# Kernel optimization log

Hardware: AMD Instinct MI355X
Metric: run time of the kernel (lower is better)

Reference implementation:

```python
import jax, jax.numpy as jnp
import numpy as np

B, S, D, H, I, E, K, L, C = 4, 1024, 512, 8, 2048, 8, 2, 4, 4
D2 = D // 2
EPS = 1e-5  # torch LayerNorm default


def _ln(x, w, b):
    m = jnp.mean(x, -1, keepdims=True)
    v = jnp.mean((x - m) ** 2, -1, keepdims=True)
    return (x - m) * jax.lax.rsqrt(v + EPS) * w + b


def setup_inputs() -> dict:
    key = jax.random.key(0)
    ks = iter(jax.random.split(key, 40))
    n = lambda shp, s=0.02: jax.random.normal(next(ks), shp, dtype=jnp.float32) * s
    return {
        'embeddings': jax.random.normal(next(ks), (B, S, D), jnp.float32),
        'attention_mask': jnp.ones((B, S), jnp.float32),
        'in_w': n((L, 3 * D, D)), 'in_b': jnp.zeros((L, 3 * D)),
        'out_w': n((L, D, D)), 'out_b': jnp.zeros((L, D)),
        'ln1_w': jnp.ones((L, D)), 'ln1_b': jnp.zeros((L, D)),
        'ln2_w': jnp.ones((L, D)), 'ln2_b': jnp.zeros((L, D)),
        'gate_w': n((L, E, D)),
        'e_w1': n((L, E, D, I)), 'e_b1': jnp.zeros((L, E, I)),
        'e_w2': n((L, E, I, D)), 'e_b2': jnp.zeros((L, E, D)),
        'mln_w': jnp.ones((L, D)), 'mln_b': jnp.zeros((L, D)),
        'fln_w': jnp.ones((D,)), 'fln_b': jnp.zeros((D,)),
        'pool_w': n((D, D)), 'pool_b': jnp.zeros((D,)),
        'cls_w': n((C, D)), 'cls_b': jnp.zeros((C,)),
        'cf_w1': n((D2, D)), 'cf_b1': jnp.zeros((D2,)),
        'cf_w2': n((1, D2)), 'cf_b2': jnp.zeros((1,)),
    }


def _forward(embeddings, attention_mask, in_w, in_b, out_w, out_b, ln1_w, ln1_b,
             ln2_w, ln2_b, gate_w, e_w1, e_b1, e_w2, e_b2, mln_w, mln_b,
             fln_w, fln_b, pool_w, pool_b, cls_w, cls_b, cf_w1, cf_b1, cf_w2, cf_b2):
    x = embeddings
    dh = D // H
    total_aux = jnp.float32(0.0)
    for l in range(L):
        # --- self-attention (eval mode, dropout off) ---
        h = _ln(x, ln1_w[l], ln1_b[l])
        qkv = h @ in_w[l].T + in_b[l]                       # (B,S,3D)
        q, k, v = jnp.split(qkv, 3, axis=-1)
        q = q.reshape(B, S, H, dh).transpose(0, 2, 1, 3)
        k = k.reshape(B, S, H, dh).transpose(0, 2, 1, 3)
        v = v.reshape(B, S, H, dh).transpose(0, 2, 1, 3)
        scores = jnp.einsum('bhqd,bhkd->bhqk', q, k) / (dh ** 0.5)
        attn = jax.nn.softmax(scores, axis=-1)
        ctx = jnp.einsum('bhqk,bhkd->bhqd', attn, v).transpose(0, 2, 1, 3).reshape(B, S, D)
        x = x + (ctx @ out_w[l].T + out_b[l])
        # --- MoE FFN (residual is the post-norm2 tensor, per source) ---
        h = _ln(x, ln2_w[l], ln2_b[l])
        flat = h.reshape(-1, D)                             # (T,D)
        probs = jax.nn.softmax(flat @ gate_w[l].T, axis=-1) # (T,E)
        vals, idx = jax.lax.top_k(probs, K)                 # (T,K)
        vals = vals / vals.sum(-1, keepdims=True)
        onehot = jax.nn.one_hot(idx, E, dtype=flat.dtype)   # (T,K,E)
        comb = jnp.einsum('tk,tke->te', vals, onehot)       # (T,E) per-expert weight, 0 if not selected
        mid = jax.nn.gelu(jnp.einsum('td,edf->tef', flat, e_w1[l]) + e_b1[l], approximate=False)
        eout = jnp.einsum('tef,efd->ted', mid, e_w2[l]) + e_b2[l]
        moe_out = jnp.einsum('ted,te->td', eout, comb).reshape(B, S, D)
        moe_out = moe_out * attention_mask[..., None]
        x = _ln(h + moe_out, mln_w[l], mln_b[l])
        usage = onehot.sum((0, 1)) / flat.shape[0]
        total_aux = total_aux + jnp.mean((usage - 1.0 / E) ** 2)
    # --- head ---
    x = _ln(x, fln_w, fln_b)
    me = attention_mask[..., None]
    pooled = (x * me).sum(1) / jnp.maximum(me.sum(1), 1e-9)
    pooled = jnp.tanh(pooled @ pool_w.T + pool_b)
    logits = pooled @ cls_w.T + cls_b
    conf = jax.nn.sigmoid(jax.nn.relu(pooled @ cf_w1.T + cf_b1) @ cf_w2.T + cf_b2)
    return logits, total_aux / L, conf


def reference(embeddings, attention_mask, in_w, in_b, out_w, out_b, ln1_w, ln1_b,
              ln2_w, ln2_b, gate_w, e_w1, e_b1, e_w2, e_b2, mln_w, mln_b,
              fln_w, fln_b, pool_w, pool_b, cls_w, cls_b, cf_w1, cf_b1, cf_w2, cf_b2):
    return _forward(embeddings, attention_mask, in_w, in_b, out_w, out_b, ln1_w, ln1_b,
                    ln2_w, ln2_b, gate_w, e_w1, e_b1, e_w2, e_b2, mln_w, mln_b,
                    fln_w, fln_b, pool_w, pool_b, cls_w, cls_b, cf_w1, cf_b1, cf_w2, cf_b2)
```

## Files before the change

kernel.cpp:

```cpp
#include <hip/hip_runtime.h>
#include <math.h>

#define B_ 4
#define S_ 1024
#define D_ 512
#define H_ 8
#define DH_ 64
#define I_ 2048
#define E_ 8
#define L_ 4
#define T_ 4096

using bf16x8 = __attribute__((ext_vector_type(8))) __bf16;
using f32x4  = __attribute__((ext_vector_type(4))) float;

typedef __attribute__((address_space(1))) const void gvoid;
typedef __attribute__((address_space(3))) void lvoid;
__device__ __forceinline__ void gl_lds16(const void* g, void* l){
  __builtin_amdgcn_global_load_lds((gvoid*)g, (lvoid*)l, 16, 0, 0);
}

__device__ __forceinline__ float wred_sum(float v){
#pragma unroll
  for(int m=32;m>0;m>>=1) v += __shfl_xor(v, m, 64);
  return v;
}
__device__ __forceinline__ unsigned short f2bf(float f){
  unsigned x = __float_as_uint(f);
  unsigned r = (x + 0x7FFFu + ((x>>16)&1u)) >> 16;
  return (unsigned short)r;
}
__device__ __forceinline__ float bf2f(unsigned short u){
  return __uint_as_float(((unsigned)u)<<16);
}
__device__ __forceinline__ unsigned pk2(float a, float b){
  return (unsigned)f2bf(a) | ((unsigned)f2bf(b)<<16);
}

template<int BM, int BN, bool MOE, bool GATHER, bool OUT_BF16, int ACT, bool ADD_IN>
__global__ __launch_bounds__(512)
void gemm_k(const unsigned short* __restrict__ A, const unsigned short* __restrict__ Bv,
            void* Cp, const float* __restrict__ bias, const float* addin,
            int M, int N, int K, int lda, int ldb, int ldc,
            int hdiv, long sAb, long sAh, long sBb, long sBh, long sCb, long sCh,
            float scale,
            const int* __restrict__ moff, const int* __restrict__ mcnt,
            const int* __restrict__ rowtok, const int* __restrict__ btab,
            long sBe, int biasStride, int nby)
{
  constexpr int BK = 64;
  constexpr int WM = BM/2, WN = BN/4, FM = WM/16, FNN = WN/16;
  constexpr int RPC = 64;
  constexpr int SHPC = 4096;
  constexpr int NA = BM/RPC, NB = BN/RPC;
  __shared__ unsigned short As[2*BM*BK];
  __shared__ unsigned short Bs[2*BN*BK];

  const int tid = threadIdx.x, wid = tid>>6, lane = tid&63;
  const int wy = wid>>2, wx = wid&3, ln16 = lane&15;

  const int nwg = gridDim.x, cpx = nwg >> 3;
  const int lin = blockIdx.x;
  const int wg  = (lin & 7)*cpx + (lin >> 3);
  const int bxi = wg / nby, byi = wg % nby;

  int m0 = bxi*BM;
  const int n0 = byi*BN;

  float* Cf = nullptr; unsigned short* Ch = nullptr;
  const float* biasp = bias;
  const unsigned short* Bp = Bv;
  int seg = 0, cnt = M;

  if constexpr (MOE){
    int tv = btab[bxi];
    if (tv < 0) return;
    int e = tv>>8;
    m0 = (tv&255)*BM;
    seg = moff[e]; cnt = mcnt[e];
    Bp = Bv + (long)e*sBe;
    if constexpr (OUT_BF16) Ch = (unsigned short*)Cp; else Cf = (float*)Cp;
    if (biasp) biasp += (long)e*biasStride;
  } else {
    int z = blockIdx.z, zb = z/hdiv, zh = z%hdiv;
    A  += (long)zb*sAb + (long)zh*sAh;
    Bp += (long)zb*sBb + (long)zh*sBh;
    long coff = (long)zb*sCb + (long)zh*sCh;
    if constexpr (OUT_BF16) Ch = (unsigned short*)Cp + coff; else Cf = ((float*)Cp) + coff;
    if constexpr (ADD_IN) addin += coff;
  }

  const int srow = tid >> 3;
  const int scol = ((tid & 7) ^ (srow & 7)) * 8;
  long ga[NA], gb[NB];
#pragma unroll
  for (int j=0; j<NA; j++){
    int r = m0 + j*RPC + srow;
    if constexpr (MOE){
      r = min(r, cnt-1);
      long gr = GATHER ? (long)rowtok[seg+r] : (long)(seg+r);
      ga[j] = gr*lda + scol;
    } else {
      ga[j] = (long)min(r, M-1)*lda + scol;
    }
  }
#pragma unroll
  for (int j=0; j<NB; j++){
    int bn = min(n0 + j*RPC + srow, N-1);
    gb[j] = (long)bn*ldb + scol;
  }

  f32x4 acc[FM][FNN];
#pragma unroll
  for(int i=0;i<FM;i++)
#pragma unroll
    for(int j=0;j<FNN;j++){ f32x4 z = {0.f,0.f,0.f,0.f}; acc[i][j] = z; }

  const int nt = K/BK;
  const int rsw = ln16 & 7;
  const int u0 = ((lane>>4)     ^ rsw) * 8;
  const int u1 = ((4+(lane>>4)) ^ rsw) * 8;

#pragma unroll
  for (int j=0; j<NA; j++) gl_lds16(A + ga[j], As + j*SHPC + wid*512);
#pragma unroll
  for (int j=0; j<NB; j++) gl_lds16(Bp + gb[j], Bs + j*SHPC + wid*512);

  for (int t = 0; t < nt; ++t){
    const int cb = t & 1;
    const unsigned short* Ab = As + cb*BM*BK;
    const unsigned short* Bb = Bs + cb*BN*BK;
    unsigned short* An = As + (cb^1)*BM*BK;
    unsigned short* Bn = Bs + (cb^1)*BN*BK;
    const bool pf = (t+1 < nt);
    const long k0n = (long)(t+1)*BK;

    asm volatile("s_waitcnt vmcnt(0)" ::: "memory");
    __builtin_amdgcn_s_barrier();
    __builtin_amdgcn_sched_barrier(0);

    if (pf){
#pragma unroll
      for (int j=0; j<NA; j++) gl_lds16(A + ga[j] + k0n, An + j*SHPC + wid*512);
    }
    {
      bf16x8 fa[FM], fb[FNN];
#pragma unroll
      for(int i=0;i<FM;i++) fa[i] = *(const bf16x8*)&Ab[(wy*WM + i*16 + ln16)*BK + u0];
#pragma unroll
      for(int j=0;j<FNN;j++) fb[j] = *(const bf16x8*)&Bb[(wx*WN + j*16 + ln16)*BK + u0];
      __builtin_amdgcn_s_setprio(1);
#pragma unroll
      for(int i=0;i<FM;i++)
#pragma unroll
        for(int j=0;j<FNN;j++)
          acc[i][j] = __builtin_amdgcn_mfma_f32_16x16x32_bf16(fa[i], fb[j], acc[i][j], 0, 0, 0);
      __builtin_amdgcn_s_setprio(0);
    }
    if (pf){
#pragma unroll
      for (int j=0; j<NB; j++) gl_lds16(Bp + gb[j] + k0n, Bn + j*SHPC + wid*512);
    }
    {
      bf16x8 fa[FM], fb[FNN];
#pragma unroll
      for(int i=0;i<FM;i++) fa[i] = *(const bf16x8*)&Ab[(wy*WM + i*16 + ln16)*BK + u1];
#pragma unroll
      for(int j=0;j<FNN;j++) fb[j] = *(const bf16x8*)&Bb[(wx*WN + j*16 + ln16)*BK + u1];
      __builtin_amdgcn_s_setprio(1);
#pragma unroll
      for(int i=0;i<FM;i++)
#pragma unroll
        for(int j=0;j<FNN;j++)
          acc[i][j] = __builtin_amdgcn_mfma_f32_16x16x32_bf16(fa[i], fb[j], acc[i][j], 0, 0, 0);
      __builtin_amdgcn_s_setprio(0);
    }
  }

#pragma unroll
  for(int i=0;i<FM;i++){
    int mbase = m0 + wy*WM + i*16 + (lane>>4)*4;
#pragma unroll
    for(int j=0;j<FNN;j++){
      int n = n0 + wx*WN + j*16 + ln16;
      float bv = biasp ? biasp[n] : 0.f;
      f32x4 v = acc[i][j];
#pragma unroll
      for(int r=0;r<4;r++){
        int m = mbase + r;
        if (m < cnt){
          float x = v[r]*scale + bv;
          if constexpr (ACT == 1) x = 0.5f*x*(1.f + erff(x*0.70710678118654752f));
          long ci = (long)(MOE ? seg + m : m)*ldc + n;
          if constexpr (ADD_IN) x += addin[ci];
          if constexpr (OUT_BF16) Ch[ci] = f2bf(x);
          else Cf[ci] = x;
        }
      }
    }
  }
}

__global__ __launch_bounds__(256)
void flash_k(const unsigned short* __restrict__ qkvb, const unsigned short* __restrict__ Vt,
             unsigned short* __restrict__ ctx)
{
  __shared__ unsigned short Pl[4][16*72];
  const int qt = blockIdx.x, z = blockIdx.y, b = z>>3, h = z&7;
  const int wid = threadIdx.x>>6, lane = threadIdx.x&63;
  const int ln16 = lane&15, g = lane>>4;
  const int q0 = qt*64 + wid*16;
  unsigned short* Pw = &Pl[wid][0];

  const unsigned short* Qp = qkvb + (long)(b*1024 + q0 + ln16)*1536 + h*64 + g*8;
  bf16x8 qf0 = *(const bf16x8*)Qp;
  bf16x8 qf1 = *(const bf16x8*)(Qp + 32);
  const unsigned short* Kbase = qkvb + (long)b*1024*1536 + 512 + h*64 + g*8;
  const unsigned short* Vbase = Vt + (long)z*65536 + g*8;

  float m_s[4], l_s[4];
  f32x4 oacc[4];
#pragma unroll
  for(int r=0;r<4;r++){ m_s[r] = -1e30f; l_s[r] = 0.f; }
#pragma unroll
  for(int j=0;j<4;j++){ f32x4 zz = {0.f,0.f,0.f,0.f}; oacc[j] = zz; }

  for (int t = 0; t < 16; ++t){
    bf16x8 kf[4][2], vf[4][2];
#pragma unroll
    for(int j=0;j<4;j++){
      const unsigned short* kp = Kbase + (long)(t*64 + j*16 + ln16)*1536;
      kf[j][0] = *(const bf16x8*)kp;
      kf[j][1] = *(const bf16x8*)(kp + 32);
      const unsigned short* vp = Vbase + (long)(j*16 + ln16)*1024 + t*64;
      vf[j][0] = *(const bf16x8*)vp;
      vf[j][1] = *(const bf16x8*)(vp + 32);
    }
    f32x4 sacc[4];
#pragma unroll
    for(int j=0;j<4;j++){ f32x4 zz = {0.f,0.f,0.f,0.f}; sacc[j] = zz; }
#pragma unroll
    for(int j=0;j<4;j++){
      sacc[j] = __builtin_amdgcn_mfma_f32_16x16x32_bf16(qf0, kf[j][0], sacc[j], 0,0,0);
      sacc[j] = __builtin_amdgcn_mfma_f32_16x16x32_bf16(qf1, kf[j][1], sacc[j], 0,0,0);
    }
#pragma unroll
    for(int j=0;j<4;j++)
#pragma unroll
      for(int r=0;r<4;r++) sacc[j][r] *= 0.125f;
    float alpha[4];
#pragma unroll
    for(int r=0;r<4;r++){
      float mx = fmaxf(fmaxf(sacc[0][r], sacc[1][r]), fmaxf(sacc[2][r], sacc[3][r]));
#pragma unroll
      for(int m=1;m<16;m<<=1) mx = fmaxf(mx, __shfl_xor(mx, m, 64));
      float mn = fmaxf(m_s[r], mx);
      alpha[r] = __expf(m_s[r] - mn);
      m_s[r] = mn;
    }
#pragma unroll
    for(int j=0;j<4;j++)
#pragma unroll
      for(int r=0;r<4;r++) sacc[j][r] = __expf(sacc[j][r] - m_s[r]);
#pragma unroll
    for(int r=0;r<4;r++){
      float rs = sacc[0][r]+sacc[1][r]+sacc[2][r]+sacc[3][r];
#pragma unroll
      for(int m=1;m<16;m<<=1) rs += __shfl_xor(rs, m, 64);
      l_s[r] = l_s[r]*alpha[r] + rs;
    }
#pragma unroll
    for(int j=0;j<4;j++)
#pragma unroll
      for(int r=0;r<4;r++) oacc[j][r] *= alpha[r];
#pragma unroll
    for(int j=0;j<4;j++)
#pragma unroll
      for(int r=0;r<4;r++)
        Pw[(g*4+r)*72 + j*16 + ln16] = f2bf(sacc[j][r]);
    bf16x8 pf0 = *(const bf16x8*)&Pw[ln16*72 + g*8];
    bf16x8 pf1 = *(const bf16x8*)&Pw[ln16*72 + 32 + g*8];
#pragma unroll
    for(int j=0;j<4;j++){
      oacc[j] = __builtin_amdgcn_mfma_f32_16x16x32_bf16(pf0, vf[j][0], oacc[j], 0,0,0);
      oacc[j] = __builtin_amdgcn_mfma_f32_16x16x32_bf16(pf1, vf[j][1], oacc[j], 0,0,0);
    }
  }
#pragma unroll
  for(int r=0;r<4;r++){
    float inv = 1.f/l_s[r];
    long row = (long)(b*1024 + q0 + g*4 + r)*512 + h*64;
#pragma unroll
    for(int j=0;j<4;j++)
      ctx[row + j*16 + ln16] = f2bf(oacc[j][r]*inv);
  }
}

template<bool OUT_BF16>
__global__ __launch_bounds__(256)
void ln_w_k(const float* __restrict__ in, const float* __restrict__ w,
            const float* __restrict__ bb, void* __restrict__ outp)
{
  int row = blockIdx.x*4 + (threadIdx.x>>6), lane = threadIdx.x&63;
  const float4* p = (const float4*)(in + (long)row*512 + lane*8);
  float4 a = p[0], c = p[1];
  float s = a.x+a.y+a.z+a.w + c.x+c.y+c.z+c.w;
  float q = a.x*a.x+a.y*a.y+a.z*a.z+a.w*a.w + c.x*c.x+c.y*c.y+c.z*c.z+c.w*c.w;
  s = wred_sum(s); q = wred_sum(q);
  float mean = s*(1.f/512.f);
  float var  = q*(1.f/512.f) - mean*mean;
  float inv  = rsqrtf(var + 1e-5f);
  const float4* wp = (const float4*)(w + lane*8);
  const float4* bp = (const float4*)(bb + lane*8);
  float4 w0 = wp[0], w1 = wp[1], b0 = bp[0], b1 = bp[1];
  float o0 = (a.x-mean)*inv*w0.x + b0.x, o1 = (a.y-mean)*inv*w0.y + b0.y;
  float o2 = (a.z-mean)*inv*w0.z + b0.z, o3 = (a.w-mean)*inv*w0.w + b0.w;
  float o4 = (c.x-mean)*inv*w1.x + b1.x, o5 = (c.y-mean)*inv*w1.y + b1.y;
  float o6 = (c.z-mean)*inv*w1.z + b1.z, o7 = (c.w-mean)*inv*w1.w + b1.w;
  if constexpr (OUT_BF16){
    *(uint4*)((unsigned short*)outp + (long)row*512 + lane*8) =
      make_uint4(pk2(o0,o1), pk2(o2,o3), pk2(o4,o5), pk2(o6,o7));
  } else {
    float4* op = (float4*)((float*)outp + (long)row*512 + lane*8);
    op[0] = make_float4(o0,o1,o2,o3);
    op[1] = make_float4(o4,o5,o6,o7);
  }
}

__global__ __launch_bounds__(256)
void ln2route_k(const float* __restrict__ in, const float* __restrict__ w,
                const float* __restrict__ bb, unsigned short* __restrict__ h2,
                const float* __restrict__ gw,
                int* __restrict__ tok_e, float* __restrict__ tok_w)
{
  int tok = blockIdx.x*4 + (threadIdx.x>>6), lane = threadIdx.x&63;
  const float4* p = (const float4*)(in + (long)tok*512 + lane*8);
  float4 a = p[0], c = p[1];
  float s = a.x+a.y+a.z+a.w + c.x+c.y+c.z+c.w;
  float q = a.x*a.x+a.y*a.y+a.z*a.z+a.w*a.w + c.x*c.x+c.y*c.y+c.z*c.z+c.w*c.w;
  s = wred_sum(s); q = wred_sum(q);
  float mean = s*(1.f/512.f);
  float var  = q*(1.f/512.f) - mean*mean;
  float inv  = rsqrtf(var + 1e-5f);
  const float4* wp = (const float4*)(w + lane*8);
  const float4* bp = (const float4*)(bb + lane*8);
  float4 w0 = wp[0], w1 = wp[1], b0 = bp[0], b1 = bp[1];
  float o[8];
  o[0] = (a.x-mean)*inv*w0.x + b0.x; o[1] = (a.y-mean)*inv*w0.y + b0.y;
  o[2] = (a.z-mean)*inv*w0.z + b0.z; o[3] = (a.w-mean)*inv*w0.w + b0.w;
  o[4] = (c.x-mean)*inv*w1.x + b1.x; o[5] = (c.y-mean)*inv*w1.y + b1.y;
  o[6] = (c.z-mean)*inv*w1.z + b1.z; o[7] = (c.w-mean)*inv*w1.w + b1.w;
  *(uint4*)(h2 + (long)tok*512 + lane*8) =
    make_uint4(pk2(o[0],o[1]), pk2(o[2],o[3]), pk2(o[4],o[5]), pk2(o[6],o[7]));
  float lg[8];
#pragma unroll
  for(int e=0;e<8;e++){
    const float4* gr = (const float4*)(gw + e*512 + lane*8);
    float4 g0 = gr[0], g1 = gr[1];
    float d = o[0]*g0.x + o[1]*g0.y + o[2]*g0.z + o[3]*g0.w
            + o[4]*g1.x + o[5]*g1.y + o[6]*g1.z + o[7]*g1.w;
    lg[e] = wred_sum(d);
  }
  if (lane == 0){
    float mx = lg[0];
#pragma unroll
    for(int e=1;e<8;e++) mx = fmaxf(mx, lg[e]);
    float pr[8];
#pragma unroll
    for(int e=0;e<8;e++) pr[e] = expf(lg[e]-mx);
    int e0 = 0; float p0 = pr[0];
#pragma unroll
    for(int e=1;e<8;e++) if (pr[e] > p0){ p0 = pr[e]; e0 = e; }
    int e1 = -1; float p1 = -1.f;
#pragma unroll
    for(int e=0;e<8;e++) if (e != e0 && pr[e] > p1){ p1 = pr[e]; e1 = e; }
    float invp = 1.f/(p0+p1);
    tok_e[2*tok] = e0; tok_e[2*tok+1] = e1;
    tok_w[2*tok] = p0*invp; tok_w[2*tok+1] = p1*invp;
  }
}

__global__ __launch_bounds__(1024)
void plan_scatter_k(const int* __restrict__ tok_e, const float* __restrict__ tok_w,
                    int* __restrict__ offs, int* __restrict__ cnts, float* __restrict__ aux,
                    int* __restrict__ btab, int* __restrict__ btab64,
                    int* __restrict__ rowtok, float* __restrict__ roww, int* __restrict__ rowof)
{
  __shared__ int hist[8];
  __shared__ int offsS[8];
  __shared__ int base[8];
  const int t = threadIdx.x;
  if (t < 8) hist[t] = 0;
  __syncthreads();
  int e[8]; float w[8];
#pragma unroll
  for (int i=0;i<8;i++){
    e[i] = tok_e[t + i*1024];
    w[i] = tok_w[t + i*1024];
    atomicAdd(&hist[e[i]], 1);
  }
  __syncthreads();
  if (t == 0){
    int o = 0, idx = 0, idx2 = 0; float a = 0.f;
    for (int ee=0; ee<8; ee++){
      offsS[ee] = o;
      int c = hist[ee];
      o += c;
      float u = (float)c*(1.f/4096.f) - 0.125f;
      a += u*u;
      int nb = (c + 127) >> 7;
      for (int j=0;j<nb;j++) btab[idx++] = (ee<<8)|j;
      int nb2 = (c + 63) >> 6;
      for (int j=0;j<nb2;j++) btab64[idx2++] = (ee<<8)|j;
    }
    while (idx < 80) btab[idx++] = -1;
    while (idx2 < 144) btab64[idx2++] = -1;
    *aux += a*(1.f/8.f);
  }
  __syncthreads();
  if (t < 8){
    cnts[t] = hist[t];
    offs[t] = offsS[t];
    base[t] = offsS[t];
  }
  __syncthreads();
#pragma unroll
  for (int i=0;i<8;i++){
    int pos = atomicAdd(&base[e[i]], 1);
    int gi = t + i*1024;
    rowtok[pos] = gi>>1;
    roww[pos] = w[i];
    rowof[gi] = pos;
  }
}

template<bool OUT2_BF16>
__global__ __launch_bounds__(256)
void ln_moe_k(const float* __restrict__ eout, const int* __restrict__ rowof,
              const float* __restrict__ roww, const float* __restrict__ mask,
              const unsigned short* __restrict__ h2,
              const float* __restrict__ w, const float* __restrict__ bb,
              float* __restrict__ outp,
              const float* __restrict__ w2, const float* __restrict__ b2,
              void* __restrict__ out2)
{
  int tok = blockIdx.x*4 + (threadIdx.x>>6), lane = threadIdx.x&63;
  int r0 = rowof[2*tok], r1 = rowof[2*tok+1];
  float w0w = roww[r0], w1w = roww[r1], mk = mask[tok];
  const float4* ap = (const float4*)(eout + (long)r0*512 + lane*8);
  const float4* bp2 = (const float4*)(eout + (long)r1*512 + lane*8);
  float4 a0 = ap[0], a1 = ap[1], c0 = bp2[0], c1 = bp2[1];
  uint4 hu = *(const uint4*)(h2 + (long)tok*512 + lane*8);
  const unsigned short* hh = (const unsigned short*)&hu;
  float v[8];
  v[0] = bf2f(hh[0]) + (a0.x*w0w + c0.x*w1w)*mk;
  v[1] = bf2f(hh[1]) + (a0.y*w0w + c0.y*w1w)*mk;
  v[2] = bf2f(hh[2]) + (a0.z*w0w + c0.z*w1w)*mk;
  v[3] = bf2f(hh[3]) + (a0.w*w0w + c0.w*w1w)*mk;
  v[4] = bf2f(hh[4]) + (a1.x*w0w + c1.x*w1w)*mk;
  v[5] = bf2f(hh[5]) + (a1.y*w0w + c1.y*w1w)*mk;
  v[6] = bf2f(hh[6]) + (a1.z*w0w + c1.z*w1w)*mk;
  v[7] = bf2f(hh[7]) + (a1.w*w0w + c1.w*w1w)*mk;
  float s = 0.f, q = 0.f;
#pragma unroll
  for(int i=0;i<8;i++){ s += v[i]; q += v[i]*v[i]; }
  s = wred_sum(s); q = wred_sum(q);
  float mean = s*(1.f/512.f);
  float var  = q*(1.f/512.f) - mean*mean;
  float inv  = rsqrtf(var + 1e-5f);
  const float4* wp = (const float4*)(w + lane*8);
  const float4* bpp = (const float4*)(bb + lane*8);
  float4 w0 = wp[0], w1 = wp[1], b0 = bpp[0], b1 = bpp[1];
  float wv[8] = {w0.x,w0.y,w0.z,w0.w,w1.x,w1.y,w1.z,w1.w};
  float bv[8] = {b0.x,b0.y,b0.z,b0.w,b1.x,b1.y,b1.z,b1.w};
  float o[8];
#pragma unroll
  for(int i=0;i<8;i++) o[i] = (v[i]-mean)*inv*wv[i]+bv[i];
  float4* op = (float4*)(outp + (long)tok*512 + lane*8);
  op[0] = make_float4(o[0], o[1], o[2], o[3]);
  op[1] = make_float4(o[4], o[5], o[6], o[7]);
  float s2 = 0.f, q2 = 0.f;
#pragma unroll
  for(int i=0;i<8;i++){ s2 += o[i]; q2 += o[i]*o[i]; }
  s2 = wred_sum(s2); q2 = wred_sum(q2);
  float mean2 = s2*(1.f/512.f);
  float var2  = q2*(1.f/512.f) - mean2*mean2;
  float inv2  = rsqrtf(var2 + 1e-5f);
  const float4* wp2 = (const float4*)(w2 + lane*8);
  const float4* bp3 = (const float4*)(b2 + lane*8);
  float4 x0 = wp2[0], x1 = wp2[1], y0 = bp3[0], y1 = bp3[1];
  float wv2[8] = {x0.x,x0.y,x0.z,x0.w,x1.x,x1.y,x1.z,x1.w};
  float bv2[8] = {y0.x,y0.y,y0.z,y0.w,y1.x,y1.y,y1.z,y1.w};
  float o2[8];
#pragma unroll
  for(int i=0;i<8;i++) o2[i] = (o[i]-mean2)*inv2*wv2[i]+bv2[i];
  if constexpr (OUT2_BF16){
    *(uint4*)((unsigned short*)out2 + (long)tok*512 + lane*8) =
      make_uint4(pk2(o2[0],o2[1]), pk2(o2[2],o2[3]), pk2(o2[4],o2[5]), pk2(o2[6],o2[7]));
  } else {
    float4* op2 = (float4*)((float*)out2 + (long)tok*512 + lane*8);
    op2[0] = make_float4(o2[0], o2[1], o2[2], o2[3]);
    op2[1] = make_float4(o2[4], o2[5], o2[6], o2[7]);
  }
}

__global__ __launch_bounds__(256)
void vt_k(const unsigned short* __restrict__ qkvb, unsigned short* __restrict__ Vt)
{
  __shared__ unsigned short tile[64][80];
  int z = blockIdx.y, b = z>>3, h = z&7;
  int t = threadIdx.x;
  int kk = t>>2, dd = (t&3)*16;
  int dd2 = t>>2, kk2 = (t&3)*16;
  for (int c = 0; c < 4; ++c){
    int k0 = (blockIdx.x*4 + c)*64;
    const unsigned short* p = qkvb + ((long)(b*1024 + k0 + kk))*1536 + 1024 + h*64 + dd;
    uint4 u0 = *(const uint4*)p, u1 = *(const uint4*)(p+8);
    __syncthreads();
    *(uint4*)&tile[kk][dd] = u0;
    *(uint4*)&tile[kk][dd+8] = u1;
    __syncthreads();
    uint4 o0, o1;
    unsigned short* s0 = (unsigned short*)&o0;
    unsigned short* s1 = (unsigned short*)&o1;
#pragma unroll
    for(int j=0;j<8;j++){ s0[j] = tile[kk2+j][dd2]; s1[j] = tile[kk2+8+j][dd2]; }
    unsigned short* o = Vt + (long)z*65536 + (long)dd2*1024 + k0 + kk2;
    *(uint4*)o = o0; *(uint4*)(o+8) = o1;
  }
}

__global__ __launch_bounds__(256)
void transpose_cast_k(const float* __restrict__ in, unsigned short* __restrict__ outp,
                      int R, int C, int ZL)
{
  __shared__ float tile[64][65];
  int t = threadIdx.x;
  int rr = t>>2, cc = (t&3)*16;
  int cc2 = t>>2, rr2 = (t&3)*16;
  int c0 = blockIdx.x*64, r0 = blockIdx.y*64;
  for (int zi = 0; zi < ZL; ++zi){
    long zoff = (long)(blockIdx.z*ZL + zi) * R * C;
    const float* pin = in + zoff + (long)(r0+rr)*C + c0 + cc;
    float4 v0=*(const float4*)pin, v1=*(const float4*)(pin+4), v2=*(const float4*)(pin+8), v3=*(const float4*)(pin+12);
    __syncthreads();
    tile[rr][cc+0]=v0.x; tile[rr][cc+1]=v0.y; tile[rr][cc+2]=v0.z; tile[rr][cc+3]=v0.w;
    tile[rr][cc+4]=v1.x; tile[rr][cc+5]=v1.y; tile[rr][cc+6]=v1.z; tile[rr][cc+7]=v1.w;
    tile[rr][cc+8]=v2.x; tile[rr][cc+9]=v2.y; tile[rr][cc+10]=v2.z; tile[rr][cc+11]=v2.w;
    tile[rr][cc+12]=v3.x; tile[rr][cc+13]=v3.y; tile[rr][cc+14]=v3.z; tile[rr][cc+15]=v3.w;
    __syncthreads();
    unsigned tmp[8];
#pragma unroll
    for(int jj=0;jj<8;jj++)
      tmp[jj] = pk2(tile[rr2+2*jj][cc2], tile[rr2+2*jj+1][cc2]);
    uint4* dst = (uint4*)(outp + zoff + (long)(c0+cc2)*R + r0 + rr2);
    dst[0] = make_uint4(tmp[0],tmp[1],tmp[2],tmp[3]);
    dst[1] = make_uint4(tmp[4],tmp[5],tmp[6],tmp[7]);
  }
}

__global__ __launch_bounds__(256)
void cast_bf16_k(const float* __restrict__ in, unsigned short* __restrict__ outp, int n8)
{
  for (int i = blockIdx.x*256 + threadIdx.x; i < n8; i += gridDim.x*256){
    const float4* p = (const float4*)(in + (long)i*8);
    float4 a = p[0], b = p[1];
    *(uint4*)(outp + (long)i*8) = make_uint4(pk2(a.x,a.y), pk2(a.z,a.w), pk2(b.x,b.y), pk2(b.z,b.w));
  }
}

__global__ __launch_bounds__(256)
void pool2_k(const float* __restrict__ h, const float* __restrict__ mask, float* __restrict__ pooled)
{
  int b = blockIdx.x, sc = blockIdx.y, t = threadIdx.x;
  float a0 = 0.f, a1 = 0.f;
  const float* mb = mask + b*1024 + sc*128;
  const float* hbase = h + ((long)b*1024 + sc*128)*512;
  for (int s = 0; s < 128; ++s){
    float mk = mb[s];
    const float* r = hbase + (long)s*512;
    a0 += r[t]*mk; a1 += r[t+256]*mk;
  }
  pooled[((b*8 + sc)*512) + t] = a0;
  pooled[((b*8 + sc)*512) + t + 256] = a1;
}

__global__ __launch_bounds__(256)
void head_final_k(const float* __restrict__ pooled, const float* __restrict__ mask,
                  const float* __restrict__ pool_w, const float* __restrict__ pool_b,
                  const float* __restrict__ cls_w, const float* __restrict__ cls_b,
                  const float* __restrict__ cf_w1, const float* __restrict__ cf_b1,
                  const float* __restrict__ cf_w2, const float* __restrict__ cf_b2,
                  const float* __restrict__ aux, float* __restrict__ out)
{
  int b = blockIdx.x, t = threadIdx.x, wid = t>>6, lane = t&63;
  __shared__ __align__(16) float pld[512];
  __shared__ __align__(16) float p2[512];
  __shared__ float red[4];
  float ds = 0.f;
  for(int s=t; s<1024; s+=256) ds += mask[b*1024 + s];
  ds = wred_sum(ds);
  if (lane==0) red[wid] = ds;
  __syncthreads();
  float denom = fmaxf(red[0]+red[1]+red[2]+red[3], 1e-9f);
  float s0 = 0.f, s1 = 0.f;
#pragma unroll
  for(int sc=0;sc<8;sc++){
    s0 += pooled[((b*8+sc)*512) + t];
    s1 += pooled[((b*8+sc)*512) + t + 256];
  }
  pld[t]     = s0/denom;
  pld[t+256] = s1/denom;
  __syncthreads();
#pragma unroll
  for(int jj=0;jj<2;jj++){
    int j = t + jj*256;
    const float4* wr = (const float4*)(pool_w + (long)j*512);
    float acc = 0.f;
    for(int i=0;i<128;i++){
      float4 w4 = wr[i]; float4 x4 = ((const float4*)pld)[i];
      acc += w4.x*x4.x + w4.y*x4.y + w4.z*x4.z + w4.w*x4.w;
    }
    p2[j] = tanhf(acc + pool_b[j]);
  }
  __syncthreads();
  if (t < 4){
    const float4* wr = (const float4*)(cls_w + (long)t*512);
    float acc = 0.f;
    for(int i=0;i<128;i++){
      float4 w4 = wr[i]; float4 x4 = ((const float4*)p2)[i];
      acc += w4.x*x4.x + w4.y*x4.y + w4.z*x4.z + w4.w*x4.w;
    }
    out[b*4 + t] = acc + cls_b[t];
  }
  {
    const float4* wr = (const float4*)(cf_w1 + (long)t*512);
    float acc = 0.f;
    for(int i=0;i<128;i++){
      float4 w4 = wr[i]; float4 x4 = ((const float4*)p2)[i];
      acc += w4.x*x4.x + w4.y*x4.y + w4.z*x4.z + w4.w*x4.w;
    }
    acc = fmaxf(acc + cf_b1[t], 0.f) * cf_w2[t];
    acc = wred_sum(acc);
    __syncthreads();
    if (lane==0) red[wid] = acc;
    __syncthreads();
    if (t == 0){
      float sum = red[0]+red[1]+red[2]+red[3];
      out[17 + b] = 1.f/(1.f + expf(-(sum + cf_b2[0])));
    }
  }
  if (b == 0 && t == 0) out[16] = aux[0]*0.25f;
}

extern "C" void kernel_launch(void* const* d_in, const int* in_sizes, int n_in,
                              void* d_out, int out_size, void* d_ws, size_t ws_size,
                              hipStream_t stream)
{
  (void)in_sizes; (void)n_in; (void)out_size;
  const float* emb    = (const float*)d_in[0];
  const float* mask   = (const float*)d_in[1];
  const float* in_w   = (const float*)d_in[2];
  const float* in_b   = (const float*)d_in[3];
  const float* out_w  = (const float*)d_in[4];
  const float* out_b  = (const float*)d_in[5];
  const float* ln1_w  = (const float*)d_in[6];
  const float* ln1_b  = (const float*)d_in[7];
  const float* ln2_w  = (const float*)d_in[8];
  const float* ln2_b  = (const float*)d_in[9];
  const float* gate_w = (const float*)d_in[10];
  const float* e_w1   = (const float*)d_in[11];
  const float* e_b1   = (const float*)d_in[12];
  const float* e_w2   = (const float*)d_in[13];
  const float* e_b2   = (const float*)d_in[14];
  const float* mln_w  = (const float*)d_in[15];
  const float* mln_b  = (const float*)d_in[16];
  const float* fln_w  = (const float*)d_in[17];
  const float* fln_b  = (const float*)d_in[18];
  const float* pool_w = (const float*)d_in[19];
  const float* pool_b = (const float*)d_in[20];
  const float* cls_w  = (const float*)d_in[21];
  const float* cls_b  = (const float*)d_in[22];
  const float* cf_w1  = (const float*)d_in[23];
  const float* cf_b1  = (const float*)d_in[24];
  const float* cf_w2  = (const float*)d_in[25];
  const float* cf_b2  = (const float*)d_in[26];
  float* out = (float*)d_out;
  char* ws = (char*)d_ws;

  const size_t MiB = 1024*1024;
  if (ws_size < 218*MiB) return;

  float*          x     = (float*)(ws + 0*MiB);
  unsigned short* hb    = (unsigned short*)(ws + 8*MiB);
  unsigned short* qkvb  = (unsigned short*)(ws + 12*MiB);
  unsigned short* ctx   = (unsigned short*)(ws + 24*MiB);
  unsigned short* Vt    = (unsigned short*)(ws + 28*MiB);
  unsigned short* mid   = (unsigned short*)(ws + 32*MiB);
  float*          eout  = (float*)(ws + 64*MiB);
  float*          fout  = (float*)(ws + 64*MiB);
  unsigned short* w1t   = (unsigned short*)(ws + 80*MiB);
  unsigned short* w2t   = (unsigned short*)(ws + 144*MiB);
  unsigned short* inwb  = (unsigned short*)(ws + 208*MiB);
  unsigned short* outwb = (unsigned short*)(ws + 214*MiB);
  char* misc = ws + 216*MiB;
  int*   counts  = (int*)(misc + 0);
  int*   offs    = (int*)(misc + 64);
  float* aux     = (float*)(misc + 128);
  int*   btab    = (int*)(misc + 256);
  int*   btab64  = (int*)(misc + 1024);
  float* pooled  = (float*)(misc + 4096);
  int*   tok_e   = (int*)(misc + 81920);
  float* tok_w   = (float*)(misc + 114688);
  int*   rowtok  = (int*)(misc + 147456);
  float* roww    = (float*)(misc + 180224);
  int*   rowof   = (int*)(misc + 212992);

  hipMemcpyAsync(x, emb, (size_t)T_*D_*4, hipMemcpyDeviceToDevice, stream);
  hipMemsetAsync(aux, 0, 4, stream);
  cast_bf16_k<<<512, 256, 0, stream>>>(in_w, inwb, L_*3*D_*D_/8);
  cast_bf16_k<<<256, 256, 0, stream>>>(out_w, outwb, L_*D_*D_/8);
  transpose_cast_k<<<dim3(I_/64, D_/64, 4), 256, 0, stream>>>(e_w1, w1t, D_, I_, 8);
  transpose_cast_k<<<dim3(D_/64, I_/64, 4), 256, 0, stream>>>(e_w2, w2t, I_, D_, 8);

  ln_w_k<true><<<T_/4, 256, 0, stream>>>(emb, ln1_w, ln1_b, hb);

  for (int l=0; l<L_; l++){
    const float* inbl  = in_b  + (size_t)l*3*D_;
    const float* outbl = out_b + (size_t)l*D_;
    const float* gwl   = gate_w + (size_t)l*E_*D_;
    const float* eb1l  = e_b1 + (size_t)l*E_*I_;
    const float* eb2l  = e_b2 + (size_t)l*E_*D_;
    const unsigned short* inwbl  = inwb + (size_t)l*3*D_*D_;
    const unsigned short* outwbl = outwb + (size_t)l*D_*D_;
    const unsigned short* w1tl = w1t + (size_t)l*E_*I_*D_;
    const unsigned short* w2tl = w2t + (size_t)l*E_*D_*I_;

    gemm_k<64,128,false,false,true,0,false><<<dim3(768,1,1), 512, 0, stream>>>(
      hb, inwbl, qkvb, inbl, nullptr, T_, 3*D_, D_, D_, D_, 3*D_,
      1, 0,0,0,0,0,0, 1.f, nullptr, nullptr, nullptr, nullptr, 0, 0, 12);
    vt_k<<<dim3(4,32), 256, 0, stream>>>(qkvb, Vt);
    flash_k<<<dim3(16,32), 256, 0, stream>>>(qkvb, Vt, ctx);
    gemm_k<64,64,false,false,false,0,true><<<dim3(512,1,1), 512, 0, stream>>>(
      ctx, outwbl, x, outbl, x, T_, D_, D_, D_, D_, D_,
      1, 0,0,0,0,0,0, 1.f, nullptr, nullptr, nullptr, nullptr, 0, 0, 8);
    ln2route_k<<<T_/4, 256, 0, stream>>>(x, ln2_w + (size_t)l*D_, ln2_b + (size_t)l*D_,
                                         hb, gwl, tok_e, tok_w);
    plan_scatter_k<<<1, 1024, 0, stream>>>(tok_e, tok_w, offs, counts, aux, btab, btab64,
                                           rowtok, roww, rowof);
    gemm_k<128,64,true,true,true,1,false><<<dim3(2272,1,1), 512, 0, stream>>>(
      hb, w1tl, mid, eb1l, nullptr, 2*T_, I_, D_, D_, D_, I_,
      1, 0,0,0,0,0,0, 1.f, offs, counts, rowtok, btab, (long)I_*D_, I_, 32);
    gemm_k<64,128,true,false,false,0,false><<<dim3(544,1,1), 512, 0, stream>>>(
      mid, w2tl, eout, eb2l, nullptr, 2*T_, D_, I_, I_, I_, D_,
      1, 0,0,0,0,0,0, 1.f, offs, counts, nullptr, btab64, (long)D_*I_, D_, 4);
    if (l < 3){
      ln_moe_k<true><<<T_/4, 256, 0, stream>>>(eout, rowof, roww, mask, hb,
                                               mln_w + (size_t)l*D_, mln_b + (size_t)l*D_, x,
                                               ln1_w + (size_t)(l+1)*D_, ln1_b + (size_t)(l+1)*D_,
                                               (void*)hb);
    } else {
      ln_moe_k<false><<<T_/4, 256, 0, stream>>>(eout, rowof, roww, mask, hb,
                                                mln_w + (size_t)l*D_, mln_b + (size_t)l*D_, x,
                                                fln_w, fln_b, (void*)fout);
    }
  }
  pool2_k<<<dim3(4,8), 256, 0, stream>>>(fout, mask, pooled);
  head_final_k<<<4, 256, 0, stream>>>(pooled, mask, pool_w, pool_b, cls_w, cls_b,
                                      cf_w1, cf_b1, cf_w2, cf_b2, aux, out);
}
```

Measured before the change: 1.294 ms.

## Fuse V transpose into QKV GEMM epilogue, drop embedding copy, widen pooling

The QKV projection GEMM now writes the V columns straight into the transposed Vt layout from its accumulators, so the separate vt_k transpose kernel and its extra pass over V are gone. The initial device-to-device copy of the embeddings into x is removed; the first layer's out-projection reads the residual from emb instead. The pooling kernel is split into 32 chunks per batch instead of 8 to use more blocks. The fused V store writes 4-element (8-byte) pieces with a large stride, which may coalesce worse than the old LDS-staged transpose.

```diff
diff --git a/kernel.cpp b/kernel.cpp
--- a/kernel.cpp
+++ b/kernel.cpp
@@ -37,7 +37,7 @@
   return (unsigned)f2bf(a) | ((unsigned)f2bf(b)<<16);
 }
 
-template<int BM, int BN, bool MOE, bool GATHER, bool OUT_BF16, int ACT, bool ADD_IN>
+template<int BM, int BN, bool MOE, bool GATHER, bool OUT_BF16, int ACT, bool ADD_IN, bool VT>
 __global__ __launch_bounds__(512)
 void gemm_k(const unsigned short* __restrict__ A, const unsigned short* __restrict__ Bv,
             void* Cp, const float* __restrict__ bias, const float* addin,
@@ -46,7 +46,7 @@
             float scale,
             const int* __restrict__ moff, const int* __restrict__ mcnt,
             const int* __restrict__ rowtok, const int* __restrict__ btab,
-            long sBe, int biasStride, int nby)
+            long sBe, int biasStride, int nby, unsigned short* __restrict__ vtp)
 {
   constexpr int BK = 64;
   constexpr int WM = BM/2, WN = BN/4, FM = WM/16, FNN = WN/16;
@@ -174,6 +174,31 @@
         for(int j=0;j<FNN;j++)
           acc[i][j] = __builtin_amdgcn_mfma_f32_16x16x32_bf16(fa[i], fb[j], acc[i][j], 0, 0, 0);
       __builtin_amdgcn_s_setprio(0);
+    }
+  }
+
+  if constexpr (VT){
+    if (n0 >= 1024){
+#pragma unroll
+      for(int i=0;i<FM;i++){
+        int mbase = m0 + wy*WM + i*16 + (lane>>4)*4;
+        int bb = mbase >> 10;
+        int k4 = mbase & 1023;
+#pragma unroll
+        for(int j=0;j<FNN;j++){
+          int n = n0 + wx*WN + j*16 + ln16;
+          float bv = biasp ? biasp[n] : 0.f;
+          int hh = (n - 1024) >> 6, dd = (n - 1024) & 63;
+          f32x4 v = acc[i][j];
+          ushort4 pkv;
+          pkv.x = f2bf(v[0]*scale + bv);
+          pkv.y = f2bf(v[1]*scale + bv);
+          pkv.z = f2bf(v[2]*scale + bv);
+          pkv.w = f2bf(v[3]*scale + bv);
+          *(ushort4*)(vtp + (long)(bb*8 + hh)*65536 + (long)dd*1024 + k4) = pkv;
+        }
+      }
+      return;
     }
   }
 
@@ -505,32 +530,6 @@
 }
 
 __global__ __launch_bounds__(256)
-void vt_k(const unsigned short* __restrict__ qkvb, unsigned short* __restrict__ Vt)
-{
-  __shared__ unsigned short tile[64][80];
-  int z = blockIdx.y, b = z>>3, h = z&7;
-  int t = threadIdx.x;
-  int kk = t>>2, dd = (t&3)*16;
-  int dd2 = t>>2, kk2 = (t&3)*16;
-  for (int c = 0; c < 4; ++c){
-    int k0 = (blockIdx.x*4 + c)*64;
-    const unsigned short* p = qkvb + ((long)(b*1024 + k0 + kk))*1536 + 1024 + h*64 + dd;
-    uint4 u0 = *(const uint4*)p, u1 = *(const uint4*)(p+8);
-    __syncthreads();
-    *(uint4*)&tile[kk][dd] = u0;
-    *(uint4*)&tile[kk][dd+8] = u1;
-    __syncthreads();
-    uint4 o0, o1;
-    unsigned short* s0 = (unsigned short*)&o0;
-    unsigned short* s1 = (unsigned short*)&o1;
-#pragma unroll
-    for(int j=0;j<8;j++){ s0[j] = tile[kk2+j][dd2]; s1[j] = tile[kk2+8+j][dd2]; }
-    unsigned short* o = Vt + (long)z*65536 + (long)dd2*1024 + k0 + kk2;
-    *(uint4*)o = o0; *(uint4*)(o+8) = o1;
-  }
-}
-
-__global__ __launch_bounds__(256)
 void transpose_cast_k(const float* __restrict__ in, unsigned short* __restrict__ outp,
                       int R, int C, int ZL)
 {
@@ -574,15 +573,15 @@
 {
   int b = blockIdx.x, sc = blockIdx.y, t = threadIdx.x;
   float a0 = 0.f, a1 = 0.f;
-  const float* mb = mask + b*1024 + sc*128;
-  const float* hbase = h + ((long)b*1024 + sc*128)*512;
-  for (int s = 0; s < 128; ++s){
+  const float* mb = mask + b*1024 + sc*32;
+  const float* hbase = h + ((long)b*1024 + sc*32)*512;
+  for (int s = 0; s < 32; ++s){
     float mk = mb[s];
     const float* r = hbase + (long)s*512;
     a0 += r[t]*mk; a1 += r[t+256]*mk;
   }
-  pooled[((b*8 + sc)*512) + t] = a0;
-  pooled[((b*8 + sc)*512) + t + 256] = a1;
+  pooled[((b*32 + sc)*512) + t] = a0;
+  pooled[((b*32 + sc)*512) + t + 256] = a1;
 }
 
 __global__ __launch_bounds__(256)
@@ -605,9 +604,9 @@
   float denom = fmaxf(red[0]+red[1]+red[2]+red[3], 1e-9f);
   float s0 = 0.f, s1 = 0.f;
 #pragma unroll
-  for(int sc=0;sc<8;sc++){
-    s0 += pooled[((b*8+sc)*512) + t];
-    s1 += pooled[((b*8+sc)*512) + t + 256];
+  for(int sc=0;sc<32;sc++){
+    s0 += pooled[((b*32+sc)*512) + t];
+    s1 += pooled[((b*32+sc)*512) + t + 256];
   }
   pld[t]     = s0/denom;
   pld[t+256] = s1/denom;
@@ -709,14 +708,13 @@
   float* aux     = (float*)(misc + 128);
   int*   btab    = (int*)(misc + 256);
   int*   btab64  = (int*)(misc + 1024);
-  float* pooled  = (float*)(misc + 4096);
   int*   tok_e   = (int*)(misc + 81920);
   float* tok_w   = (float*)(misc + 114688);
   int*   rowtok  = (int*)(misc + 147456);
   float* roww    = (float*)(misc + 180224);
   int*   rowof   = (int*)(misc + 212992);
-
-  hipMemcpyAsync(x, emb, (size_t)T_*D_*4, hipMemcpyDeviceToDevice, stream);
+  float* pooled  = (float*)(misc + 262144);
+
   hipMemsetAsync(aux, 0, 4, stream);
   cast_bf16_k<<<512, 256, 0, stream>>>(in_w, inwb, L_*3*D_*D_/8);
   cast_bf16_k<<<256, 256, 0, stream>>>(out_w, outwb, L_*D_*D_/8);
@@ -736,24 +734,23 @@
     const unsigned short* w1tl = w1t + (size_t)l*E_*I_*D_;
     const unsigned short* w2tl = w2t + (size_t)l*E_*D_*I_;
 
-    gemm_k<64,128,false,false,true,0,false><<<dim3(768,1,1), 512, 0, stream>>>(
+    gemm_k<64,128,false,false,true,0,false,true><<<dim3(768,1,1), 512, 0, stream>>>(
       hb, inwbl, qkvb, inbl, nullptr, T_, 3*D_, D_, D_, D_, 3*D_,
-      1, 0,0,0,0,0,0, 1.f, nullptr, nullptr, nullptr, nullptr, 0, 0, 12);
-    vt_k<<<dim3(4,32), 256, 0, stream>>>(qkvb, Vt);
+      1, 0,0,0,0,0,0, 1.f, nullptr, nullptr, nullptr, nullptr, 0, 0, 12, Vt);
     flash_k<<<dim3(16,32), 256, 0, stream>>>(qkvb, Vt, ctx);
-    gemm_k<64,64,false,false,false,0,true><<<dim3(512,1,1), 512, 0, stream>>>(
-      ctx, outwbl, x, outbl, x, T_, D_, D_, D_, D_, D_,
-      1, 0,0,0,0,0,0, 1.f, nullptr, nullptr, nullptr, nullptr, 0, 0, 8);
+    gemm_k<64,64,false,false,false,0,true,false><<<dim3(512,1,1), 512, 0, stream>>>(
+      ctx, outwbl, x, outbl, (l == 0 ? emb : x), T_, D_, D_, D_, D_, D_,
+      1, 0,0,0,0,0,0, 1.f, nullptr, nullptr, nullptr, nullptr, 0, 0, 8, nullptr);
     ln2route_k<<<T_/4, 256, 0, stream>>>(x, ln2_w + (size_t)l*D_, ln2_b + (size_t)l*D_,
                                          hb, gwl, tok_e, tok_w);
     plan_scatter_k<<<1, 1024, 0, stream>>>(tok_e, tok_w, offs, counts, aux, btab, btab64,
                                            rowtok, roww, rowof);
-    gemm_k<128,64,true,true,true,1,false><<<dim3(2272,1,1), 512, 0, stream>>>(
+    gemm_k<128,64,true,true,true,1,false,false><<<dim3(2272,1,1), 512, 0, stream>>>(
       hb, w1tl, mid, eb1l, nullptr, 2*T_, I_, D_, D_, D_, I_,
-      1, 0,0,0,0,0,0, 1.f, offs, counts, rowtok, btab, (long)I_*D_, I_, 32);
-    gemm_k<64,128,true,false,false,0,false><<<dim3(544,1,1), 512, 0, stream>>>(
+      1, 0,0,0,0,0,0, 1.f, offs, counts, rowtok, btab, (long)I_*D_, I_, 32, nullptr);
+    gemm_k<64,128,true,false,false,0,false,false><<<dim3(544,1,1), 512, 0, stream>>>(
       mid, w2tl, eout, eb2l, nullptr, 2*T_, D_, I_, I_, I_, D_,
-      1, 0,0,0,0,0,0, 1.f, offs, counts, nullptr, btab64, (long)D_*I_, D_, 4);
+      1, 0,0,0,0,0,0, 1.f, offs, counts, nullptr, btab64, (long)D_*I_, D_, 4, nullptr);
     if (l < 3){
       ln_moe_k<true><<<T_/4, 256, 0, stream>>>(eout, rowof, roww, mask, hb,
                                                mln_w + (size_t)l*D_, mln_b + (size_t)l*D_, x,
@@ -765,7 +762,7 @@
                                                 fln_w, fln_b, (void*)fout);
     }
   }
-  pool2_k<<<dim3(4,8), 256, 0, stream>>>(fout, mask, pooled);
+  pool2_k<<<dim3(4,32), 256, 0, stream>>>(fout, mask, pooled);
   head_final_k<<<4, 256, 0, stream>>>(pooled, mask, pool_w, pool_b, cls_w, cls_b,
                                       cf_w1, cf_b1, cf_w2, cf_b2, aux, out);
 }
```

After: 1.257 ms. -2.8%, faster.
